# Kernel optimization log

Measured on AMD Instinct MI355X. Metric: run time of the kernel, lower is better.

The kernel has to match this reference:

```python
import jax, jax.numpy as jnp
import numpy as np
import math

C = 1.0           # curvature magnitude (ball = Stereographic(-c))
B = 256; H = 256; IN = 256   # batch must equal hidden_size (broadcasting in original source)
EPS = 1e-15
BALL_EPS = 4e-3   # geoopt float32 projection eps

def _norm(x):
    return jnp.linalg.norm(x, axis=-1, keepdims=True)

def _project(x, c=C):
    # geoopt projects results of mobius ops back into the open ball
    maxn = (1.0 - BALL_EPS) / math.sqrt(c)
    n = jnp.maximum(_norm(x), EPS)
    return jnp.where(n > maxn, x * (maxn / n), x)

def _mobius_add(x, y, c=C):
    x2 = jnp.sum(x * x, -1, keepdims=True)
    y2 = jnp.sum(y * y, -1, keepdims=True)
    xy = jnp.sum(x * y, -1, keepdims=True)
    num = (1.0 + 2.0 * c * xy + c * y2) * x + (1.0 - c * x2) * y
    den = 1.0 + 2.0 * c * xy + c * c * x2 * y2
    return _project(num / jnp.maximum(den, EPS), c)

def _expmap0(u, c=C):
    sc = math.sqrt(c)
    n = jnp.maximum(_norm(u), EPS)
    return _project(jnp.tanh(sc * n) * u / (sc * n), c)

def _logmap0(y, c=C):
    sc = math.sqrt(c)
    n = jnp.maximum(_norm(y), EPS)
    t = jnp.arctanh(jnp.clip(sc * n, 0.0, 1.0 - 1e-7))
    return t * y / (sc * n)

def _mobius_pw_mul(w, x, c=C):
    # geoopt mobius_pointwise_mul(w, x): tan_k(|w*x|/|x| * artan_k(|x|)) * (w*x)/|w*x|
    sc = math.sqrt(c)
    wx = w * x
    xn = jnp.maximum(_norm(x), EPS)
    wxn = jnp.maximum(_norm(wx), EPS)
    t = jnp.arctanh(jnp.clip(sc * xn, 0.0, 1.0 - 1e-7))
    return _project(jnp.tanh(wxn / xn * t) * wx / (sc * wxn), c)

def _mlr(x, z, r, c=C):
    # x:[B,D] ball points; z:[Cc,D]; r:[Cc,1]; B == Cc (required by original broadcasting)
    sc = math.sqrt(c)
    a = z / jnp.cosh(r * sc) ** 2                      # [Cc,D]
    u = r[None, :, :] * z[:, None, :]                  # [Cc,B,D]; q[cl,b]=expmap0(r[b]*z[cl]) as in source
    q = _expmap0(u, c)
    px = _mobius_add(-q, x[None, :, :], c)             # [Cc,B,D]
    lam = 2.0 / (1.0 - jnp.sum(px * px, -1))           # [Cc,B]
    na = jnp.linalg.norm(a, axis=-1)                   # [Cc]
    a_unit = a / jnp.maximum(na[:, None], 1e-12)       # F.normalize eps
    dot = jnp.einsum('cbd,cd->cb', px, a_unit)
    logits = 2.0 * na[:, None] * jnp.arcsinh(dot * lam)
    return logits.T                                     # [B,Cc]

def _fc(x, z, r, c=C):
    sc = math.sqrt(c)
    w = jnp.sinh(_mlr(x, z, r, c) * sc)                # [B,Cc]
    # torch broadcasts the [B] scale along the LAST axis (B==Cc)
    scale = jnp.sqrt(c * jnp.sum(w * w, -1)) + 1.0     # [B]
    return scale[None, :] * w

def _cell(hyp_x, hidden, Wz_z, Wz_r, Uz_z, Uz_r, Wr_z, Wr_r, Ur_z, Ur_r,
          Wh_z, Wh_r, Uh_z, Uh_r, b_z, b_r, b_h):
    z = _mobius_add(_mobius_add(_fc(hidden, Wz_z, Wz_r), _fc(hyp_x, Uz_z, Uz_r)), b_z)
    z = jax.nn.sigmoid(_logmap0(z))
    r = _mobius_add(_mobius_add(_fc(hidden, Wr_z, Wr_r), _fc(hyp_x, Ur_z, Ur_r)), b_r)
    r = jax.nn.sigmoid(_logmap0(r))
    r_point_h = _mobius_pw_mul(hidden, r)
    # NOTE: in the original source this value is computed then immediately overwritten
    _dead = _mobius_add(_fc(r_point_h, Wh_z, Wh_r), _fc(hyp_x, Uh_z, Uh_r))
    h_tilde = _mobius_add(r, b_h)
    minus_h_oplus_htilde = _mobius_add(-hidden, h_tilde)
    return _mobius_add(hidden, _mobius_pw_mul(minus_h_oplus_htilde, z))


def setup_inputs() -> dict:
    key = jax.random.key(0)
    ks = jax.random.split(key, 18)
    def ball(k, shape, scale=0.3):
        v = jax.random.normal(k, shape, dtype=jnp.float32)
        return v * (scale / (1.0 + jnp.linalg.norm(v, axis=-1, keepdims=True)))
    def zp(k, out_d, in_d):
        return jax.random.uniform(k, (out_d, in_d), minval=-0.05, maxval=0.05, dtype=jnp.float32)
    def rp(k, out_d):
        return jax.random.uniform(k, (out_d, 1), minval=-1.0, maxval=1.0, dtype=jnp.float32)
    return {
        'hyp_x': ball(ks[0], (B, IN)),
        'hidden': ball(ks[1], (B, H)),
        'Wz_z': zp(ks[2], H, H), 'Wz_r': rp(ks[3], H),
        'Uz_z': zp(ks[4], H, IN), 'Uz_r': rp(ks[5], H),
        'Wr_z': zp(ks[6], H, H), 'Wr_r': rp(ks[7], H),
        'Ur_z': zp(ks[8], H, IN), 'Ur_r': rp(ks[9], H),
        'Wh_z': zp(ks[10], H, H), 'Wh_r': rp(ks[11], H),
        'Uh_z': zp(ks[12], H, IN), 'Uh_r': rp(ks[13], H),
        'b_z': ball(ks[14], (H,), 0.05),
        'b_r': ball(ks[15], (H,), 0.05),
        'b_h': ball(ks[16], (H,), 0.05),
    }


def reference(hyp_x, hidden, Wz_z, Wz_r, Uz_z, Uz_r, Wr_z, Wr_r, Ur_z, Ur_r,
              Wh_z, Wh_r, Uh_z, Uh_r, b_z, b_r, b_h):
    return _cell(hyp_x, hidden, Wz_z, Wz_r, Uz_z, Uz_r, Wr_z, Wr_r, Ur_z, Ur_r,
                 Wh_z, Wh_r, Uh_z, Uh_r, b_z, b_r, b_h)
```

## Files before the change

### kernel.cpp

```cpp
#include <hip/hip_runtime.h>
#include <math.h>

#define EPSF 1e-15f


__device__ __forceinline__ float f_rcp(float x){ return __builtin_amdgcn_rcpf(x); }
__device__ __forceinline__ float f_tanh(float x){
    float e = __expf(2.f * x);
    return 1.f - 2.f * f_rcp(e + 1.f);
}
__device__ __forceinline__ float f_sinh(float x){
    float e = __expf(x);
    return 0.5f * (e - f_rcp(e));
}
__device__ __forceinline__ float f_cosh(float x){
    float e = __expf(x);
    return 0.5f * (e + f_rcp(e));
}
__device__ __forceinline__ float f_asinh(float x){
    float ax = fabsf(x);
    float r = __logf(ax + sqrtf(fmaf(ax, ax, 1.f)));
    return copysignf(r, x);
}
__device__ __forceinline__ float f_artanh(float x){
    return 0.5f * __logf((1.f + x) * f_rcp(1.f - x));
}
__device__ __forceinline__ float f_sigmoid(float x){
    return f_rcp(1.f + __expf(-x));
}

__device__ __forceinline__ float wredsum(float v){
    #pragma unroll
    for (int o = 32; o > 0; o >>= 1) v += __shfl_xor(v, o);
    return v;
}
__device__ __forceinline__ void wredsum3(float& a, float& b, float& c){
    #pragma unroll
    for (int o = 32; o > 0; o >>= 1){
        a += __shfl_xor(a, o);
        b += __shfl_xor(b, o);
        c += __shfl_xor(c, o);
    }
}

__device__ __forceinline__ float fc_elem(float M, float nzc, float nac, float rb, float x2b){
    const float maxn = 1.0f - 4e-3f;
    float d  = M * f_rcp(nzc);
    float tq = f_tanh(rb * nzc);
    if (fabsf(tq) > maxn) tq = copysignf(maxn, tq);
    float A    = fmaf(-2.f*tq, d, 1.f + x2b);
    float den  = fmaxf(fmaf(tq*tq, x2b, fmaf(-2.f*tq, d, 1.f)), EPSF);
    float rden = f_rcp(den);
    float alpha = -tq * A * rden;
    float beta  = (1.f - tq*tq) * rden;
    float dot   = fmaf(beta, d, alpha);
    float pxn2  = fmaxf(alpha*alpha + 2.f*alpha*beta*d + beta*beta*x2b, 0.f);
    float n = fmaxf(sqrtf(pxn2), EPSF);
    if (n > maxn){
        dot *= maxn * f_rcp(n);
        pxn2 = maxn * maxn;
    }
    float lam = 2.f * f_rcp(1.f - pxn2);
    return f_sinh(2.f * nac * f_asinh(dot * lam));
}

__global__ __launch_bounds__(256) void fc_kernel(
    const float* __restrict__ hidden, const float* __restrict__ hyp_x,
    const float* __restrict__ Wz_z, const float* __restrict__ Uz_z,
    const float* __restrict__ Wr_z, const float* __restrict__ Ur_z,
    const float* __restrict__ Wz_r, const float* __restrict__ Uz_r,
    const float* __restrict__ Wr_r, const float* __restrict__ Ur_r,
    float* __restrict__ ws)
{
    __shared__ float As[32][260];
    __shared__ float Bs[32][260];
    __shared__ float nz_s[32], na_s[32], x2_s[32], Sred[32];

    const int bid   = blockIdx.x;
    const int mat   = bid >> 6;
    const int tile  = bid & 63;
    const int ctile = tile >> 3;
    const int cbase = ctile * 32;
    const int bbase = (tile & 7) * 32;

    const float* Z  = (mat==0) ? Wz_z : (mat==1) ? Uz_z : (mat==2) ? Wr_z : Ur_z;
    const float* Rv = (mat==0) ? Wz_r : (mat==1) ? Uz_r : (mat==2) ? Wr_r : Ur_r;
    const float* X  = (mat==0 || mat==2) ? hidden : hyp_x;

    const int t  = threadIdx.x;
    const int tc = t >> 4, tb = t & 15;

    #pragma unroll 4
    for (int q = 0; q < 8; ++q){
        int f   = q*256 + t;
        int row = f >> 6;
        int col = (f & 63) * 4;
        *(float4*)&As[row][col] = *(const float4*)(Z + (cbase+row)*256 + col);
        *(float4*)&Bs[row][col] = *(const float4*)(X + (bbase+row)*256 + col);
    }
    __syncthreads();

    float sa = 0.f, sb = 0.f;
    {
        int r = t >> 3, seg = t & 7;
        #pragma unroll 2
        for (int q = 0; q < 8; ++q){
            float4 a = *(const float4*)&As[r][seg*32 + q*4];
            float4 b = *(const float4*)&Bs[r][seg*32 + q*4];
            sa += a.x*a.x + a.y*a.y + a.z*a.z + a.w*a.w;
            sb += b.x*b.x + b.y*b.y + b.z*b.z + b.w*b.w;
        }
    }
    sa += __shfl_xor(sa, 1); sb += __shfl_xor(sb, 1);
    sa += __shfl_xor(sa, 2); sb += __shfl_xor(sb, 2);
    sa += __shfl_xor(sa, 4); sb += __shfl_xor(sb, 4);
    if ((t & 7) == 0){
        int r = t >> 3;
        float nzv = fmaxf(sqrtf(sa), EPSF);
        nz_s[r] = nzv;
        float ch = f_cosh(Rv[cbase + r]);
        na_s[r] = nzv * f_rcp(ch*ch);
        x2_s[r] = sb;
    }
    if (t < 32) Sred[t] = 0.f;

    float acc00 = 0.f, acc01 = 0.f, acc10 = 0.f, acc11 = 0.f;
    #pragma unroll 4
    for (int k = 0; k < 256; k += 4){
        float4 a0 = *(const float4*)&As[tc][k];
        float4 a1 = *(const float4*)&As[tc+16][k];
        float4 b0 = *(const float4*)&Bs[tb][k];
        float4 b1 = *(const float4*)&Bs[tb+16][k];
        acc00 += a0.x*b0.x + a0.y*b0.y + a0.z*b0.z + a0.w*b0.w;
        acc01 += a0.x*b1.x + a0.y*b1.y + a0.z*b1.z + a0.w*b1.w;
        acc10 += a1.x*b0.x + a1.y*b0.y + a1.z*b0.z + a1.w*b0.w;
        acc11 += a1.x*b1.x + a1.y*b1.y + a1.z*b1.z + a1.w*b1.w;
    }
    __syncthreads();

    const int c0 = cbase + tc, c1 = cbase + tc + 16;
    const int b0 = bbase + tb, b1 = bbase + tb + 16;
    float nz0 = nz_s[tc],   nz1 = nz_s[tc+16];
    float na0 = na_s[tc],   na1 = na_s[tc+16];
    float x20 = x2_s[tb],   x21 = x2_s[tb+16];
    float r0  = Rv[b0],     r1  = Rv[b1];

    float w00 = fc_elem(acc00, nz0, na0, r0, x20);
    float w01 = fc_elem(acc01, nz0, na0, r1, x21);
    float w10 = fc_elem(acc10, nz1, na1, r0, x20);
    float w11 = fc_elem(acc11, nz1, na1, r1, x21);

    float* Wout = ws + mat * 65536;
    Wout[b0*256 + c0] = w00;
    Wout[b1*256 + c0] = w01;
    Wout[b0*256 + c1] = w10;
    Wout[b1*256 + c1] = w11;

    atomicAdd(&Sred[tb],      w00*w00 + w10*w10);
    atomicAdd(&Sred[tb+16],   w01*w01 + w11*w11);
    __syncthreads();
    if (t < 32) ws[262144 + mat*2048 + ctile*256 + bbase + t] = Sred[t];
}

__device__ __forceinline__ float mobius_add4(const float x[4], const float y[4], float res[4]){
    float x2 = 0.f, y2 = 0.f, xy = 0.f;
    #pragma unroll
    for (int k = 0; k < 4; ++k){ x2 += x[k]*x[k]; y2 += y[k]*y[k]; xy += x[k]*y[k]; }
    wredsum3(x2, y2, xy);
    float cA  = 1.f + 2.f*xy + y2;
    float cB  = 1.f - x2;
    float rden = f_rcp(fmaxf(1.f + 2.f*xy + x2*y2, EPSF));
    float n2  = 0.f;
    #pragma unroll
    for (int k = 0; k < 4; ++k){ res[k] = (cA*x[k] + cB*y[k]) * rden; n2 += res[k]*res[k]; }
    n2 = wredsum(n2);
    float n = fmaxf(sqrtf(n2), EPSF);
    const float maxn = 1.0f - 4e-3f;
    if (n > maxn){
        float s = maxn * f_rcp(n);
        #pragma unroll
        for (int k = 0; k < 4; ++k) res[k] *= s;
        n = maxn;
    }
    return n;
}

__device__ __forceinline__ void load_G(const float* __restrict__ ws, int mat, int b, int c4, float dst[4]){
    const float* Wm = ws + mat*65536;
    float4 g = *(const float4*)(Wm + b*256 + c4);
    const float* Sp = ws + 262144 + mat*2048;
    float s0 = 0.f, s1 = 0.f, s2 = 0.f, s3 = 0.f;
    #pragma unroll 2
    for (int ct = 0; ct < 8; ++ct){
        float4 sp = *(const float4*)(Sp + ct*256 + c4);
        s0 += sp.x; s1 += sp.y; s2 += sp.z; s3 += sp.w;
    }
    dst[0] = (sqrtf(s0) + 1.f) * g.x;
    dst[1] = (sqrtf(s1) + 1.f) * g.y;
    dst[2] = (sqrtf(s2) + 1.f) * g.z;
    dst[3] = (sqrtf(s3) + 1.f) * g.w;
}

__global__ __launch_bounds__(256) void cell_kernel(
    const float* __restrict__ hidden,
    const float* __restrict__ b_z, const float* __restrict__ b_r, const float* __restrict__ b_h,
    const float* __restrict__ ws, float* __restrict__ out)
{
    const int b    = blockIdx.x * 4 + (threadIdx.x >> 6);
    const int lane = threadIdx.x & 63;
    const int c4   = lane * 4;
    const float maxn = 1.0f - 4e-3f;

    float h[4], u[4], v[4], t1[4], pre[4], zv[4], rv[4], ht[4], tmp[4], pw[4], mh[4];

    { float4 hv = *(const float4*)(hidden + b*256 + c4);
      h[0]=hv.x; h[1]=hv.y; h[2]=hv.z; h[3]=hv.w; }

    load_G(ws, 0, b, c4, u);
    load_G(ws, 1, b, c4, v);
    mobius_add4(u, v, t1);
    { float4 bb = *(const float4*)(b_z + c4); tmp[0]=bb.x; tmp[1]=bb.y; tmp[2]=bb.z; tmp[3]=bb.w; }
    float n  = mobius_add4(t1, tmp, pre);
    float sc = f_artanh(fminf(n, 1.f - 1e-7f)) * f_rcp(n);
    #pragma unroll
    for (int k = 0; k < 4; ++k) zv[k] = f_sigmoid(pre[k]*sc);

    load_G(ws, 2, b, c4, u);
    load_G(ws, 3, b, c4, v);
    mobius_add4(u, v, t1);
    { float4 bb = *(const float4*)(b_r + c4); tmp[0]=bb.x; tmp[1]=bb.y; tmp[2]=bb.z; tmp[3]=bb.w; }
    n  = mobius_add4(t1, tmp, pre);
    sc = f_artanh(fminf(n, 1.f - 1e-7f)) * f_rcp(n);
    #pragma unroll
    for (int k = 0; k < 4; ++k) rv[k] = f_sigmoid(pre[k]*sc);

    { float4 bb = *(const float4*)(b_h + c4); tmp[0]=bb.x; tmp[1]=bb.y; tmp[2]=bb.z; tmp[3]=bb.w; }
    mobius_add4(rv, tmp, ht);

    #pragma unroll
    for (int k = 0; k < 4; ++k) tmp[k] = -h[k];
    mobius_add4(tmp, ht, mh);

    float xn2 = 0.f, wxn2 = 0.f, dum = 0.f;
    #pragma unroll
    for (int k = 0; k < 4; ++k){ tmp[k] = mh[k]*zv[k]; xn2 += zv[k]*zv[k]; wxn2 += tmp[k]*tmp[k]; }
    wredsum3(xn2, wxn2, dum);
    float xn  = fmaxf(sqrtf(xn2),  EPSF);
    float wxn = fmaxf(sqrtf(wxn2), EPSF);
    float th  = f_tanh(wxn * f_rcp(xn) * f_artanh(fminf(xn, 1.f - 1e-7f)));
    float coef = th * f_rcp(wxn);
    if (th > maxn) coef *= maxn * f_rcp(th);
    #pragma unroll
    for (int k = 0; k < 4; ++k) pw[k] = coef * tmp[k];

    mobius_add4(h, pw, tmp);
    float4 o; o.x = tmp[0]; o.y = tmp[1]; o.z = tmp[2]; o.w = tmp[3];
    *(float4*)(out + b*256 + c4) = o;
}

extern "C" void kernel_launch(void* const* d_in, const int* in_sizes, int n_in,
                              void* d_out, int out_size, void* d_ws, size_t ws_size,
                              hipStream_t stream) {
    (void)in_sizes; (void)n_in; (void)out_size; (void)ws_size;
    const float* hyp_x  = (const float*)d_in[0];
    const float* hidden = (const float*)d_in[1];
    const float* Wz_z   = (const float*)d_in[2];
    const float* Wz_r   = (const float*)d_in[3];
    const float* Uz_z   = (const float*)d_in[4];
    const float* Uz_r   = (const float*)d_in[5];
    const float* Wr_z   = (const float*)d_in[6];
    const float* Wr_r   = (const float*)d_in[7];
    const float* Ur_z   = (const float*)d_in[8];
    const float* Ur_r   = (const float*)d_in[9];
    const float* b_z    = (const float*)d_in[14];
    const float* b_r    = (const float*)d_in[15];
    const float* b_h    = (const float*)d_in[16];
    float* ws  = (float*)d_ws;
    float* out = (float*)d_out;

    fc_kernel<<<dim3(256), dim3(256), 0, stream>>>(
        hidden, hyp_x, Wz_z, Uz_z, Wr_z, Ur_z, Wz_r, Uz_r, Wr_r, Ur_r, ws);
    cell_kernel<<<dim3(64), dim3(256), 0, stream>>>(
        hidden, b_z, b_r, b_h, ws, out);
}
```

Before: 102.4 us.

## Split FC matmuls over K and move norms and elementwise work to separate kernels

Splits each hyperbolic FC matmul across eight K-slices with 64x64 output tiles, writing partial products to workspace. Row norms are computed by dedicated blocks. A new finish kernel sums the partials, applies the elementwise FC transform and per-row squared sums, and the cell kernel reads these directly. The aim is to fill more compute units than the 256-block launch did, at the cost of an extra launch and much more partial-sum global traffic.

```diff
diff --git a/kernel.cpp b/kernel.cpp
--- a/kernel.cpp
+++ b/kernel.cpp
@@ -3,6 +3,13 @@
 
 #define EPSF 1e-15f
 
+
+#define MPART 0
+#define NZOFF 2097152
+#define NAOFF 2098176
+#define X2OFF 2099200
+#define SROFF 2099712
+#define WOFF  2100736
 
 __device__ __forceinline__ float f_rcp(float x){ return __builtin_amdgcn_rcpf(x); }
 __device__ __forceinline__ float f_tanh(float x){
@@ -64,7 +71,7 @@
     return f_sinh(2.f * nac * f_asinh(dot * lam));
 }
 
-__global__ __launch_bounds__(256) void fc_kernel(
+__global__ __launch_bounds__(256) void mm_norm_kernel(
     const float* __restrict__ hidden, const float* __restrict__ hyp_x,
     const float* __restrict__ Wz_z, const float* __restrict__ Uz_z,
     const float* __restrict__ Wr_z, const float* __restrict__ Ur_z,
@@ -72,94 +79,142 @@
     const float* __restrict__ Wr_r, const float* __restrict__ Ur_r,
     float* __restrict__ ws)
 {
-    __shared__ float As[32][260];
-    __shared__ float Bs[32][260];
-    __shared__ float nz_s[32], na_s[32], x2_s[32], Sred[32];
-
-    const int bid   = blockIdx.x;
-    const int mat   = bid >> 6;
-    const int tile  = bid & 63;
-    const int ctile = tile >> 3;
-    const int cbase = ctile * 32;
-    const int bbase = (tile & 7) * 32;
-
-    const float* Z  = (mat==0) ? Wz_z : (mat==1) ? Uz_z : (mat==2) ? Wr_z : Ur_z;
-    const float* Rv = (mat==0) ? Wz_r : (mat==1) ? Uz_r : (mat==2) ? Wr_r : Ur_r;
-    const float* X  = (mat==0 || mat==2) ? hidden : hyp_x;
-
-    const int t  = threadIdx.x;
-    const int tc = t >> 4, tb = t & 15;
-
-    #pragma unroll 4
-    for (int q = 0; q < 8; ++q){
-        int f   = q*256 + t;
-        int row = f >> 6;
-        int col = (f & 63) * 4;
-        *(float4*)&As[row][col] = *(const float4*)(Z + (cbase+row)*256 + col);
-        *(float4*)&Bs[row][col] = *(const float4*)(X + (bbase+row)*256 + col);
-    }
-    __syncthreads();
-
-    float sa = 0.f, sb = 0.f;
-    {
-        int r = t >> 3, seg = t & 7;
+    __shared__ float smem[4608];
+    const int bid = blockIdx.x;
+    const int t   = threadIdx.x;
+
+    if (bid < 512){
+        const int mat   = bid >> 7;
+        const int rest  = bid & 127;
+        const int tile  = rest >> 3;
+        const int ks    = rest & 7;
+        const int cbase = (tile >> 2) * 64;
+        const int bbase = (tile & 3) * 64;
+        const int k0    = ks * 32;
+
+        const float* Z = (mat==0) ? Wz_z : (mat==1) ? Uz_z : (mat==2) ? Wr_z : Ur_z;
+        const float* X = ((mat & 1) == 0) ? hidden : hyp_x;
+
+        float* As = smem;
+        float* Bs = smem + 2304;
+
+        #pragma unroll
+        for (int q = 0; q < 2; ++q){
+            int slot = q*256 + t;
+            int row  = slot >> 3;
+            int col  = (slot & 7) * 4;
+            *(float4*)&As[row*36 + col] = *(const float4*)(Z + (cbase+row)*256 + k0 + col);
+            *(float4*)&Bs[row*36 + col] = *(const float4*)(X + (bbase+row)*256 + k0 + col);
+        }
+        __syncthreads();
+
+        const int tc = t >> 4, tb = t & 15;
+        float acc[4][4];
+        #pragma unroll
+        for (int i = 0; i < 4; ++i)
+            #pragma unroll
+            for (int j = 0; j < 4; ++j) acc[i][j] = 0.f;
+
         #pragma unroll 2
-        for (int q = 0; q < 8; ++q){
-            float4 a = *(const float4*)&As[r][seg*32 + q*4];
-            float4 b = *(const float4*)&Bs[r][seg*32 + q*4];
-            sa += a.x*a.x + a.y*a.y + a.z*a.z + a.w*a.w;
-            sb += b.x*b.x + b.y*b.y + b.z*b.z + b.w*b.w;
-        }
-    }
-    sa += __shfl_xor(sa, 1); sb += __shfl_xor(sb, 1);
-    sa += __shfl_xor(sa, 2); sb += __shfl_xor(sb, 2);
-    sa += __shfl_xor(sa, 4); sb += __shfl_xor(sb, 4);
-    if ((t & 7) == 0){
-        int r = t >> 3;
-        float nzv = fmaxf(sqrtf(sa), EPSF);
-        nz_s[r] = nzv;
-        float ch = f_cosh(Rv[cbase + r]);
-        na_s[r] = nzv * f_rcp(ch*ch);
-        x2_s[r] = sb;
-    }
-    if (t < 32) Sred[t] = 0.f;
-
-    float acc00 = 0.f, acc01 = 0.f, acc10 = 0.f, acc11 = 0.f;
-    #pragma unroll 4
-    for (int k = 0; k < 256; k += 4){
-        float4 a0 = *(const float4*)&As[tc][k];
-        float4 a1 = *(const float4*)&As[tc+16][k];
-        float4 b0 = *(const float4*)&Bs[tb][k];
-        float4 b1 = *(const float4*)&Bs[tb+16][k];
-        acc00 += a0.x*b0.x + a0.y*b0.y + a0.z*b0.z + a0.w*b0.w;
-        acc01 += a0.x*b1.x + a0.y*b1.y + a0.z*b1.z + a0.w*b1.w;
-        acc10 += a1.x*b0.x + a1.y*b0.y + a1.z*b0.z + a1.w*b0.w;
-        acc11 += a1.x*b1.x + a1.y*b1.y + a1.z*b1.z + a1.w*b1.w;
-    }
-    __syncthreads();
-
-    const int c0 = cbase + tc, c1 = cbase + tc + 16;
-    const int b0 = bbase + tb, b1 = bbase + tb + 16;
-    float nz0 = nz_s[tc],   nz1 = nz_s[tc+16];
-    float na0 = na_s[tc],   na1 = na_s[tc+16];
-    float x20 = x2_s[tb],   x21 = x2_s[tb+16];
-    float r0  = Rv[b0],     r1  = Rv[b1];
-
-    float w00 = fc_elem(acc00, nz0, na0, r0, x20);
-    float w01 = fc_elem(acc01, nz0, na0, r1, x21);
-    float w10 = fc_elem(acc10, nz1, na1, r0, x20);
-    float w11 = fc_elem(acc11, nz1, na1, r1, x21);
-
-    float* Wout = ws + mat * 65536;
-    Wout[b0*256 + c0] = w00;
-    Wout[b1*256 + c0] = w01;
-    Wout[b0*256 + c1] = w10;
-    Wout[b1*256 + c1] = w11;
-
-    atomicAdd(&Sred[tb],      w00*w00 + w10*w10);
-    atomicAdd(&Sred[tb+16],   w01*w01 + w11*w11);
-    __syncthreads();
-    if (t < 32) ws[262144 + mat*2048 + ctile*256 + bbase + t] = Sred[t];
+        for (int kc = 0; kc < 8; ++kc){
+            int k = kc * 4;
+            float4 a0 = *(const float4*)&As[(tc     )*36 + k];
+            float4 a1 = *(const float4*)&As[(tc + 16)*36 + k];
+            float4 a2 = *(const float4*)&As[(tc + 32)*36 + k];
+            float4 a3 = *(const float4*)&As[(tc + 48)*36 + k];
+            float4 b0 = *(const float4*)&Bs[(tb     )*36 + k];
+            float4 b1 = *(const float4*)&Bs[(tb + 16)*36 + k];
+            float4 b2 = *(const float4*)&Bs[(tb + 32)*36 + k];
+            float4 b3 = *(const float4*)&Bs[(tb + 48)*36 + k];
+            const float4 av[4] = {a0,a1,a2,a3};
+            const float4 bv[4] = {b0,b1,b2,b3};
+            #pragma unroll
+            for (int i = 0; i < 4; ++i)
+                #pragma unroll
+                for (int j = 0; j < 4; ++j){
+                    acc[i][j] += av[i].x*bv[j].x + av[i].y*bv[j].y
+                               + av[i].z*bv[j].z + av[i].w*bv[j].w;
+                }
+        }
+        __syncthreads();
+
+        float* Ts = smem;
+        #pragma unroll
+        for (int i = 0; i < 4; ++i)
+            #pragma unroll
+            for (int j = 0; j < 4; ++j)
+                Ts[(tb + 16*j)*65 + (tc + 16*i)] = acc[i][j];
+        __syncthreads();
+
+        float* Mp = ws + MPART + ((mat*8 + ks) << 16);
+        const int bl = t >> 2;
+        const int cs = (t & 3) * 4;
+        #pragma unroll
+        for (int s = 0; s < 4; ++s){
+            float4 v;
+            v.x = Ts[bl*65 + cs + 16*s + 0];
+            v.y = Ts[bl*65 + cs + 16*s + 1];
+            v.z = Ts[bl*65 + cs + 16*s + 2];
+            v.w = Ts[bl*65 + cs + 16*s + 3];
+            *(float4*)(Mp + (bbase + bl)*256 + (cbase + cs + 16*s)) = v;
+        }
+    } else {
+        const int wv   = t >> 6;
+        const int lane = t & 63;
+        const int g    = (bid - 512)*4 + wv;
+        const int src  = g >> 8;
+        const int row  = g & 255;
+        const float* sp = (src==0) ? Wz_z : (src==1) ? Uz_z : (src==2) ? Wr_z
+                        : (src==3) ? Ur_z : (src==4) ? hidden : hyp_x;
+        float4 v = *(const float4*)(sp + row*256 + lane*4);
+        float s = v.x*v.x + v.y*v.y + v.z*v.z + v.w*v.w;
+        s = wredsum(s);
+        if (lane == 0){
+            if (src < 4){
+                float nz = fmaxf(sqrtf(s), EPSF);
+                ws[NZOFF + src*256 + row] = nz;
+                const float* rv = (src==0) ? Wz_r : (src==1) ? Uz_r : (src==2) ? Wr_r : Ur_r;
+                float ch = f_cosh(rv[row]);
+                ws[NAOFF + src*256 + row] = nz * f_rcp(ch*ch);
+            } else {
+                ws[X2OFF + (src-4)*256 + row] = s;
+            }
+        }
+    }
+}
+
+__global__ __launch_bounds__(256) void fc_finish_kernel(
+    const float* __restrict__ Wz_r, const float* __restrict__ Uz_r,
+    const float* __restrict__ Wr_r, const float* __restrict__ Ur_r,
+    float* __restrict__ ws)
+{
+    const int b    = blockIdx.x * 4 + (threadIdx.x >> 6);
+    const int lane = threadIdx.x & 63;
+    const int c4   = lane * 4;
+
+    #pragma unroll
+    for (int m = 0; m < 4; ++m){
+        const float* Mp = ws + MPART + ((m*8) << 16) + b*256 + c4;
+        float4 M = *(const float4*)Mp;
+        #pragma unroll
+        for (int ks = 1; ks < 8; ++ks){
+            float4 p = *(const float4*)(Mp + (ks << 16));
+            M.x += p.x; M.y += p.y; M.z += p.z; M.w += p.w;
+        }
+        float4 nz = *(const float4*)(ws + NZOFF + m*256 + c4);
+        float4 na = *(const float4*)(ws + NAOFF + m*256 + c4);
+        const float* rv = (m==0) ? Wz_r : (m==1) ? Uz_r : (m==2) ? Wr_r : Ur_r;
+        float rb  = rv[b];
+        float x2b = ws[X2OFF + (m & 1)*256 + b];
+        float4 w;
+        w.x = fc_elem(M.x, nz.x, na.x, rb, x2b);
+        w.y = fc_elem(M.y, nz.y, na.y, rb, x2b);
+        w.z = fc_elem(M.z, nz.z, na.z, rb, x2b);
+        w.w = fc_elem(M.w, nz.w, na.w, rb, x2b);
+        float S = wredsum(w.x*w.x + w.y*w.y + w.z*w.z + w.w*w.w);
+        *(float4*)(ws + WOFF + m*65536 + b*256 + c4) = w;
+        if (lane == 0) ws[SROFF + m*256 + b] = S;
+    }
 }
 
 __device__ __forceinline__ float mobius_add4(const float x[4], const float y[4], float res[4]){
@@ -183,22 +238,6 @@
         n = maxn;
     }
     return n;
-}
-
-__device__ __forceinline__ void load_G(const float* __restrict__ ws, int mat, int b, int c4, float dst[4]){
-    const float* Wm = ws + mat*65536;
-    float4 g = *(const float4*)(Wm + b*256 + c4);
-    const float* Sp = ws + 262144 + mat*2048;
-    float s0 = 0.f, s1 = 0.f, s2 = 0.f, s3 = 0.f;
-    #pragma unroll 2
-    for (int ct = 0; ct < 8; ++ct){
-        float4 sp = *(const float4*)(Sp + ct*256 + c4);
-        s0 += sp.x; s1 += sp.y; s2 += sp.z; s3 += sp.w;
-    }
-    dst[0] = (sqrtf(s0) + 1.f) * g.x;
-    dst[1] = (sqrtf(s1) + 1.f) * g.y;
-    dst[2] = (sqrtf(s2) + 1.f) * g.z;
-    dst[3] = (sqrtf(s3) + 1.f) * g.w;
 }
 
 __global__ __launch_bounds__(256) void cell_kernel(
@@ -211,31 +250,37 @@
     const int c4   = lane * 4;
     const float maxn = 1.0f - 4e-3f;
 
-    float h[4], u[4], v[4], t1[4], pre[4], zv[4], rv[4], ht[4], tmp[4], pw[4], mh[4];
-
+    float G[4][4];
+    #pragma unroll
+    for (int m = 0; m < 4; ++m){
+        float4 w  = *(const float4*)(ws + WOFF  + m*65536 + b*256 + c4);
+        float4 Sr = *(const float4*)(ws + SROFF + m*256 + c4);
+        G[m][0] = (sqrtf(Sr.x) + 1.f) * w.x;
+        G[m][1] = (sqrtf(Sr.y) + 1.f) * w.y;
+        G[m][2] = (sqrtf(Sr.z) + 1.f) * w.z;
+        G[m][3] = (sqrtf(Sr.w) + 1.f) * w.w;
+    }
+
+    float h[4], t1[4], pre[4], zv[4], rv4[4], ht[4], tmp[4], pw[4], mh[4];
     { float4 hv = *(const float4*)(hidden + b*256 + c4);
       h[0]=hv.x; h[1]=hv.y; h[2]=hv.z; h[3]=hv.w; }
 
-    load_G(ws, 0, b, c4, u);
-    load_G(ws, 1, b, c4, v);
-    mobius_add4(u, v, t1);
+    mobius_add4(G[0], G[1], t1);
     { float4 bb = *(const float4*)(b_z + c4); tmp[0]=bb.x; tmp[1]=bb.y; tmp[2]=bb.z; tmp[3]=bb.w; }
     float n  = mobius_add4(t1, tmp, pre);
     float sc = f_artanh(fminf(n, 1.f - 1e-7f)) * f_rcp(n);
     #pragma unroll
     for (int k = 0; k < 4; ++k) zv[k] = f_sigmoid(pre[k]*sc);
 
-    load_G(ws, 2, b, c4, u);
-    load_G(ws, 3, b, c4, v);
-    mobius_add4(u, v, t1);
+    mobius_add4(G[2], G[3], t1);
     { float4 bb = *(const float4*)(b_r + c4); tmp[0]=bb.x; tmp[1]=bb.y; tmp[2]=bb.z; tmp[3]=bb.w; }
     n  = mobius_add4(t1, tmp, pre);
     sc = f_artanh(fminf(n, 1.f - 1e-7f)) * f_rcp(n);
     #pragma unroll
-    for (int k = 0; k < 4; ++k) rv[k] = f_sigmoid(pre[k]*sc);
+    for (int k = 0; k < 4; ++k) rv4[k] = f_sigmoid(pre[k]*sc);
 
     { float4 bb = *(const float4*)(b_h + c4); tmp[0]=bb.x; tmp[1]=bb.y; tmp[2]=bb.z; tmp[3]=bb.w; }
-    mobius_add4(rv, tmp, ht);
+    mobius_add4(rv4, tmp, ht);
 
     #pragma unroll
     for (int k = 0; k < 4; ++k) tmp[k] = -h[k];
@@ -278,8 +323,10 @@
     float* ws  = (float*)d_ws;
     float* out = (float*)d_out;
 
-    fc_kernel<<<dim3(256), dim3(256), 0, stream>>>(
+    mm_norm_kernel<<<dim3(896), dim3(256), 0, stream>>>(
         hidden, hyp_x, Wz_z, Uz_z, Wr_z, Ur_z, Wz_r, Uz_r, Wr_r, Ur_r, ws);
+    fc_finish_kernel<<<dim3(64), dim3(256), 0, stream>>>(
+        Wz_r, Uz_r, Wr_r, Ur_r, ws);
     cell_kernel<<<dim3(64), dim3(256), 0, stream>>>(
         hidden, b_z, b_r, b_h, ws, out);
 }
```

Measured after the change: 107.2 us. 1.05x slower.
